# Optimization experiments

Measured on AMD Instinct MI355X. Metric: run time of the kernel, lower is better.

Reference implementation:

```python
import jax, jax.numpy as jnp
import numpy as np


def setup_inputs() -> dict:
    key = jax.random.key(0)
    k1, k2 = jax.random.split(key)
    B, L1, L2, D = 64, 1024, 1024, 768
    sent = jax.random.normal(k1, (B, L1, D), dtype=jnp.float32)
    e = jax.random.normal(k2, (B, L2, L1), dtype=jnp.float32)
    return {"sent": sent, "e": e}


def reference(sent, e):
    # Stable softmax over last axis (alignment weights over L1),
    # then weighted pooling of sent: equivalent to es @ sent.
    es = jax.nn.softmax(e, axis=-1)              # [B, L2, L1]
    out = jnp.einsum('bql,bld->bqd', es, sent)   # [B, L2, D]
    return out
```

## Files before the change

kernel.cpp:

```cpp
#include <hip/hip_runtime.h>
#include <hip/hip_bf16.h>


#define B_  64
#define L1_ 1024
#define L2_ 1024
#define D_  768

typedef __attribute__((ext_vector_type(8))) short short8;
typedef __attribute__((ext_vector_type(4))) float f32x4;
typedef __attribute__((ext_vector_type(8))) unsigned short ushort8;
typedef __attribute__((ext_vector_type(4))) unsigned short ushort4v;

static __device__ __forceinline__ unsigned short f2bf(float x) {
  union { float f; unsigned int u; } c; c.f = x;
  unsigned int r = c.u + 0x7FFF + ((c.u >> 16) & 1);
  return (unsigned short)(r >> 16);
}

#define GLOAD(gp, lp) \
  __builtin_amdgcn_global_load_lds((const __attribute__((address_space(1))) char*)(gp), \
                                   (__attribute__((address_space(3))) char*)(lp), 16, 0, 0)

__global__ __launch_bounds__(256) void transpose_cast_kernel(const float* __restrict__ sent,
                                                             unsigned short* __restrict__ sT) {
  __shared__ unsigned short tile[64][66];
  const int b  = blockIdx.z;
  const int l0 = blockIdx.y << 6;
  const int d0 = blockIdx.x << 6;
  const int t  = threadIdx.x;
  const float* sp = sent + ((size_t)b * L1_ + l0) * D_ + d0;
  const int c4 = (t & 15) << 2;
  const int r0 = t >> 4;
#pragma unroll
  for (int p = 0; p < 4; ++p) {
    const int r = r0 + (p << 4);
    float4 v = *reinterpret_cast<const float4*>(sp + (size_t)r * D_ + c4);
    tile[r][c4 + 0] = f2bf(v.x);
    tile[r][c4 + 1] = f2bf(v.y);
    tile[r][c4 + 2] = f2bf(v.z);
    tile[r][c4 + 3] = f2bf(v.w);
  }
  __syncthreads();
  unsigned short* op = sT + ((size_t)b * D_ + d0) * L1_ + l0;
  const int l8  = (t & 7) << 3;
  const int dd0 = t >> 3;
#pragma unroll
  for (int p = 0; p < 2; ++p) {
    const int d = dd0 + (p << 5);
    ushort8 w;
#pragma unroll
    for (int j = 0; j < 8; ++j) w[j] = tile[l8 + j][d];
    *reinterpret_cast<ushort8*>(op + (size_t)d * L1_ + l8) = w;
  }
}

__global__ __launch_bounds__(256) void exp_rows_kernel(const float* __restrict__ e,
                                                       unsigned short* __restrict__ expE,
                                                       float* __restrict__ rsInv) {
  const int t    = threadIdx.x;
  const int lane = t & 63;
  const int wv   = t >> 6;
  const int rowb = blockIdx.x << 4;
#pragma unroll
  for (int i = 0; i < 4; ++i) {
    const int row = rowb + (i << 2) + wv;
    const float* rp = e + (size_t)row * L1_;
    unsigned short* op = expE + (size_t)row * L1_;
    float s = 0.f;
#pragma unroll
    for (int j = 0; j < 4; ++j) {
      float4 v = *reinterpret_cast<const float4*>(rp + j * 256 + lane * 4);
      float e0 = __expf(v.x), e1 = __expf(v.y), e2 = __expf(v.z), e3 = __expf(v.w);
      s += (e0 + e1) + (e2 + e3);
      ushort4v o;
      o[0] = f2bf(e0); o[1] = f2bf(e1); o[2] = f2bf(e2); o[3] = f2bf(e3);
      *reinterpret_cast<ushort4v*>(op + j * 256 + lane * 4) = o;
    }
#pragma unroll
    for (int dd = 1; dd < 64; dd <<= 1) s += __shfl_xor(s, dd);
    if (lane == 0) rsInv[row] = 1.0f / s;
  }
}

#define BM2 256
#define BN2 256
#define BK2 64
#define NT2   (L1_ / BK2)
#define MT2   (L2_ / BM2)
#define NTL2  (D_ / BN2)
#define NWG2  (B_ * MT2 * NTL2)

#define SAU(T, BUF, RR) do { const int _tt = (T) & (NT2 - 1); \
    GLOAD(Asrc2 + (size_t)(RR) * 64 * L1_ + _tt * BK2, \
          &As2[BUF][((RR) * 64 + w * 8) * BK2]); \
    GLOAD(Asrc2 + (size_t)((RR) + 2) * 64 * L1_ + _tt * BK2, \
          &As2[BUF][(((RR) + 2) * 64 + w * 8) * BK2]); \
  } while (0)
#define SBU(T, BUF, RR) do { const int _tt = (T) & (NT2 - 1); \
    GLOAD(Bsrc2 + (size_t)(RR) * 64 * L1_ + _tt * BK2, \
          &Bs2[BUF][((RR) * 64 + w * 8) * BK2]); \
    GLOAD(Bsrc2 + (size_t)((RR) + 1) * 64 * L1_ + _tt * BK2, \
          &Bs2[BUF][(((RR) + 1) * 64 + w * 8) * BK2]); \
  } while (0)

#define PHASE2(RB, RH, KH, PRE, POST) do { \
    PRE \
    short8 a_[4], b_[4]; \
    _Pragma("unroll") \
    for (int ii = 0; ii < 4; ++ii) { \
      const int ra_ = wm * 128 + ((RH) * 4 + ii) * 16 + l15; \
      a_[ii] = *reinterpret_cast<const short8*>( \
          &As2[RB][ra_ * BK2 + ((((KH) * 4 + ksl) ^ (l15 & 7)) << 3)]); \
      const int rb_ = wn * 64 + ii * 16 + l15; \
      b_[ii] = *reinterpret_cast<const short8*>( \
          &Bs2[RB][rb_ * BK2 + ((((KH) * 4 + ksl) ^ (l15 & 7)) << 3)]); \
    } \
    __builtin_amdgcn_sched_barrier(0); \
    __builtin_amdgcn_s_barrier(); \
    asm volatile("s_waitcnt lgkmcnt(0)" ::: "memory"); \
    __builtin_amdgcn_sched_barrier(0); \
    __builtin_amdgcn_s_setprio(1); \
    _Pragma("unroll") \
    for (int ii = 0; ii < 4; ++ii) \
      _Pragma("unroll") \
      for (int jj = 0; jj < 4; ++jj) \
        acc[(RH) * 4 + ii][jj] = __builtin_amdgcn_mfma_f32_16x16x32_bf16( \
            a_[ii], b_[jj], acc[(RH) * 4 + ii][jj], 0, 0, 0); \
    __builtin_amdgcn_s_setprio(0); \
    POST \
    __builtin_amdgcn_sched_barrier(0); \
    __builtin_amdgcn_s_barrier(); \
  } while (0)

#define TILE2(T, RB, SBUF) do { \
    PHASE2(RB, 0, 0, SAU((T) + 1, SBUF, 1);, ;); \
    PHASE2(RB, 0, 1, SBU((T) + 1, SBUF, 0);, ;); \
    PHASE2(RB, 1, 0, SBU((T) + 1, SBUF, 2); SAU((T) + 2, RB, 0);, ;); \
    PHASE2(RB, 1, 1, ;, \
        asm volatile("s_waitcnt vmcnt(2)" ::: "memory"); \
        __builtin_amdgcn_sched_barrier(0);); \
  } while (0)

__global__ __launch_bounds__(512, 2) void gemm2_kernel(const unsigned short* __restrict__ expE,
                                                       const unsigned short* __restrict__ sT,
                                                       const float* __restrict__ rsInv,
                                                       float* __restrict__ out) {
  __shared__ __align__(16) unsigned short As2[2][BM2 * BK2];
  __shared__ __align__(16) unsigned short Bs2[2][BN2 * BK2];
  __shared__ float sArr[BM2];

  const int orig = blockIdx.x;
  const int wgid = (orig & 7) * (NWG2 / 8) + (orig >> 3);
  const int b    = wgid / (MT2 * NTL2);
  const int rem  = wgid % (MT2 * NTL2);
  const int m0   = (rem / NTL2) * BM2;
  const int n0   = (rem % NTL2) * BN2;

  const int t    = threadIdx.x;
  const int lane = t & 63;
  const int w    = t >> 6;
  const int wm   = w >> 2;
  const int wn   = w & 3;
  const int l15  = lane & 15;
  const int ksl  = lane >> 4;

  const int srow  = w * 8 + (lane >> 3);
  const int sslot = (lane & 7) ^ (lane >> 3);
  const unsigned short* Asrc2 = expE + ((size_t)b * L2_ + m0 + srow) * L1_ + sslot * 8;
  const unsigned short* Bsrc2 = sT   + ((size_t)b * D_  + n0 + srow) * L1_ + sslot * 8;

  f32x4 acc[8][4] = {};

  if (t < BM2) sArr[t] = rsInv[(size_t)b * L2_ + m0 + t];
  SAU(0, 0, 0); SAU(0, 0, 1); SBU(0, 0, 0); SBU(0, 0, 2);
  SAU(1, 1, 0);
  asm volatile("s_waitcnt vmcnt(2) lgkmcnt(0)" ::: "memory");
  __builtin_amdgcn_s_barrier();
  __builtin_amdgcn_sched_barrier(0);

#pragma unroll 1
  for (int kt = 0; kt < NT2; kt += 2) {
    TILE2(kt,     0, 1);
    TILE2(kt + 1, 1, 0);
  }

  const int rbase = (lane >> 4) << 2;
  float* Cb = out + ((size_t)b * L2_ + m0 + wm * 128) * D_ + n0 + wn * 64;
#pragma unroll
  for (int i = 0; i < 8; ++i) {
    float inv[4];
#pragma unroll
    for (int r = 0; r < 4; ++r)
      inv[r] = sArr[wm * 128 + i * 16 + rbase + r];
#pragma unroll
    for (int jj = 0; jj < 4; ++jj)
#pragma unroll
      for (int r = 0; r < 4; ++r)
        Cb[(size_t)(i * 16 + rbase + r) * D_ + jj * 16 + l15] = acc[i][jj][r] * inv[r];
  }
}

#define BM 128
#define BN 256
#define BK 32
#define NT    (L1_ / BK)
#define NTILE (D_ / BN)
#define MTILE (L2_ / BM)
#define NWG   (NTILE * MTILE * B_)

#define SW(r) ((((r) >> 2) ^ (r)) & 3)

#define LOADA(T) do { const int _ta = (T) & (NT - 1);                                        \
    aregs[0] = *reinterpret_cast<const float4*>(Ae + (size_t)rA * L1_ + _ta * BK + cA);      \
    aregs[1] = *reinterpret_cast<const float4*>(Ae + (size_t)rA * L1_ + _ta * BK + cA + 4);  \
  } while (0)

#define EXPWRITE(T) do { if ((T) < NT) {                                        \
    unsigned short* Ad_ = &As[(T) & 1][0];                                      \
    float ex_[8];                                                               \
    ex_[0] = __expf(aregs[0].x); ex_[1] = __expf(aregs[0].y);                   \
    ex_[2] = __expf(aregs[0].z); ex_[3] = __expf(aregs[0].w);                   \
    ex_[4] = __expf(aregs[1].x); ex_[5] = __expf(aregs[1].y);                   \
    ex_[6] = __expf(aregs[1].z); ex_[7] = __expf(aregs[1].w);                   \
    psum += ((ex_[0] + ex_[1]) + (ex_[2] + ex_[3]))                             \
          + ((ex_[4] + ex_[5]) + (ex_[6] + ex_[7]));                            \
    ushort8 w0_;                                                                \
    _Pragma("unroll")                                                           \
    for (int q_ = 0; q_ < 8; ++q_) w0_[q_] = f2bf(ex_[q_]);                     \
    *reinterpret_cast<ushort8*>(&Ad_[rA * BK + aslot * 8]) = w0_;               \
  } } while (0)

#define SB(T) do { if ((T) < NT) {                                              \
    GLOAD(Bb + (size_t)rB0 * L1_ + (T) * BK + sB0, &Bs[(T) & 1][(w * 32) * BK]);      \
    GLOAD(Bb + (size_t)rB1 * L1_ + (T) * BK + sB1, &Bs[(T) & 1][(w * 32 + 16) * BK]); \
  } } while (0)

__global__ __launch_bounds__(512, 2) void gemm_fused_kernel(const float* __restrict__ e,
                                                            const unsigned short* __restrict__ sT,
                                                            float* __restrict__ out) {
  __shared__ __align__(16) unsigned short As[2][BM * BK];
  __shared__ __align__(16) unsigned short Bs[2][BN * BK];
  __shared__ float sArr[BM];

  const int orig = blockIdx.x;
  const int wgid = (orig & 7) * (NWG / 8) + (orig >> 3);
  const int b    = wgid / (NTILE * MTILE);
  const int rem  = wgid % (NTILE * MTILE);
  const int m0   = (rem / NTILE) * BM;
  const int n0   = (rem % NTILE) * BN;

  const int t    = threadIdx.x;
  const int lane = t & 63;
  const int w    = t >> 6;
  const int wm   = w >> 2;
  const int wn   = w & 3;
  const int l15  = lane & 15;
  const int ksl  = lane >> 4;
  const int rA   = w * 16 + (lane >> 2);
  const int cA   = (lane & 3) * 8;
  const int aslot = (lane & 3) ^ SW(rA);
  const int rB0  = w * 32 + (lane >> 2);
  const int rB1  = rB0 + 16;
  const int sB0  = ((lane & 3) ^ SW(rB0)) * 8;
  const int sB1  = ((lane & 3) ^ SW(rB1)) * 8;

  const float*          Ae = e  + ((size_t)b * L2_ + m0) * L1_;
  const unsigned short* Bb = sT + ((size_t)b * D_  + n0) * L1_;

  f32x4 acc[4][4] = {};
  float4 aregs[2];
  float psum = 0.f;

  LOADA(0);
  SB(0);
  EXPWRITE(0);
  LOADA(1);
  asm volatile("s_waitcnt vmcnt(2) lgkmcnt(0)" ::: "memory");
  __builtin_amdgcn_s_barrier();
  __builtin_amdgcn_sched_barrier(0);

  for (int kt = 0; kt < NT; ++kt) {
    SB(kt + 1);
    EXPWRITE(kt + 1);
    LOADA(kt + 2);

    const unsigned short* Apt = As[kt & 1];
    const unsigned short* Bpt = Bs[kt & 1];
    short8 a[4], bb[4];
    __builtin_amdgcn_s_setprio(1);
#pragma unroll
    for (int i = 0; i < 4; ++i) {
      const int ra = wm * 64 + i * 16 + l15;
      a[i] = *reinterpret_cast<const short8*>(&Apt[ra * BK + ((ksl ^ SW(ra)) << 3)]);
      const int rb = wn * 64 + i * 16 + l15;
      bb[i] = *reinterpret_cast<const short8*>(&Bpt[rb * BK + ((ksl ^ SW(rb)) << 3)]);
    }
#pragma unroll
    for (int i = 0; i < 4; ++i)
#pragma unroll
      for (int jn = 0; jn < 4; ++jn)
        acc[i][jn] = __builtin_amdgcn_mfma_f32_16x16x32_bf16(a[i], bb[jn], acc[i][jn], 0, 0, 0);
    __builtin_amdgcn_s_setprio(0);

    if (kt < NT - 1) {
      asm volatile("s_waitcnt vmcnt(2) lgkmcnt(0)" ::: "memory");
      __builtin_amdgcn_s_barrier();
      __builtin_amdgcn_sched_barrier(0);
    }
  }

  psum += __shfl_xor(psum, 1);
  psum += __shfl_xor(psum, 2);
  if ((lane & 3) == 0) sArr[rA] = psum;
  __syncthreads();

  const int rbase = (lane >> 4) << 2;
  float* Cb = out + ((size_t)b * L2_ + m0 + wm * 64) * D_ + n0 + wn * 64;
#pragma unroll
  for (int i = 0; i < 4; ++i) {
    float inv[4];
#pragma unroll
    for (int r = 0; r < 4; ++r)
      inv[r] = 1.0f / sArr[wm * 64 + i * 16 + rbase + r];
#pragma unroll
    for (int jn = 0; jn < 4; ++jn)
#pragma unroll
      for (int r = 0; r < 4; ++r)
        Cb[(size_t)(i * 16 + rbase + r) * D_ + jn * 16 + l15] = acc[i][jn][r] * inv[r];
  }
}

extern "C" void kernel_launch(void* const* d_in, const int* in_sizes, int n_in,
                              void* d_out, int out_size, void* d_ws, size_t ws_size,
                              hipStream_t stream) {
  const float* sent = (const float*)d_in[0];
  const float* e    = (const float*)d_in[1];
  float* out = (float*)d_out;

  const size_t ST_BYTES   = (size_t)B_ * D_ * L1_ * 2;
  const size_t EXPE_BYTES = (size_t)B_ * L2_ * L1_ * 2;
  const size_t RS_BYTES   = (size_t)B_ * L2_ * 4;

  unsigned short* sT = (unsigned short*)d_ws;

  transpose_cast_kernel<<<dim3(D_ / 64, L1_ / 64, B_), 256, 0, stream>>>(sent, sT);

  if (ws_size >= ST_BYTES + EXPE_BYTES + RS_BYTES) {
    unsigned short* expE  = (unsigned short*)((char*)d_ws + ST_BYTES);
    float*          rsInv = (float*)((char*)d_ws + ST_BYTES + EXPE_BYTES);
    exp_rows_kernel<<<dim3(B_ * L2_ / 16), 256, 0, stream>>>(e, expE, rsInv);
    gemm2_kernel<<<dim3(NWG2), 512, 0, stream>>>(expE, sT, rsInv, out);
  } else {
    gemm_fused_kernel<<<dim3(NWG), 512, 0, stream>>>(e, sT, out);
  }
}
```

Before: 302.5 us.

## Merge prep kernels into one launch and restructure GEMM main-loop pipeline

New measurement: 289.4 us. 1.05x faster.

```diff
diff --git a/kernel.cpp b/kernel.cpp
--- a/kernel.cpp
+++ b/kernel.cpp
@@ -21,6 +21,198 @@
 #define GLOAD(gp, lp) \
   __builtin_amdgcn_global_load_lds((const __attribute__((address_space(1))) char*)(gp), \
                                    (__attribute__((address_space(3))) char*)(lp), 16, 0, 0)
+
+#define TC_BLOCKS (12 * 16 * 64)
+__global__ __launch_bounds__(256) void prep_kernel(const float* __restrict__ sent,
+                                                   const float* __restrict__ e,
+                                                   unsigned short* __restrict__ sT,
+                                                   unsigned short* __restrict__ expE,
+                                                   float* __restrict__ rsInv) {
+  __shared__ unsigned short tile[64][66];
+  const int bid = blockIdx.x;
+  const int t   = threadIdx.x;
+  if (bid < TC_BLOCKS) {
+    const int b  = bid / 192;
+    const int r2 = bid % 192;
+    const int l0 = (r2 / 12) << 6;
+    const int d0 = (r2 % 12) << 6;
+    const float* sp = sent + ((size_t)b * L1_ + l0) * D_ + d0;
+    const int c4 = (t & 15) << 2;
+    const int r0 = t >> 4;
+#pragma unroll
+    for (int p = 0; p < 4; ++p) {
+      const int r = r0 + (p << 4);
+      float4 v = *reinterpret_cast<const float4*>(sp + (size_t)r * D_ + c4);
+      tile[r][c4 + 0] = f2bf(v.x);
+      tile[r][c4 + 1] = f2bf(v.y);
+      tile[r][c4 + 2] = f2bf(v.z);
+      tile[r][c4 + 3] = f2bf(v.w);
+    }
+    __syncthreads();
+    unsigned short* op = sT + ((size_t)b * D_ + d0) * L1_ + l0;
+    const int l8  = (t & 7) << 3;
+    const int dd0 = t >> 3;
+#pragma unroll
+    for (int p = 0; p < 2; ++p) {
+      const int d = dd0 + (p << 5);
+      ushort8 w;
+#pragma unroll
+      for (int j = 0; j < 8; ++j) w[j] = tile[l8 + j][d];
+      *reinterpret_cast<ushort8*>(op + (size_t)d * L1_ + l8) = w;
+    }
+  } else {
+    const int lane = t & 63;
+    const int wv   = t >> 6;
+    const int rowb = (bid - TC_BLOCKS) << 4;
+#pragma unroll
+    for (int i = 0; i < 4; ++i) {
+      const int row = rowb + (i << 2) + wv;
+      const float* rp = e + (size_t)row * L1_;
+      unsigned short* op = expE + (size_t)row * L1_;
+      float s = 0.f;
+#pragma unroll
+      for (int j = 0; j < 4; ++j) {
+        float4 v = *reinterpret_cast<const float4*>(rp + j * 256 + lane * 4);
+        float e0 = __expf(v.x), e1 = __expf(v.y), e2 = __expf(v.z), e3 = __expf(v.w);
+        s += (e0 + e1) + (e2 + e3);
+        ushort4v o;
+        o[0] = f2bf(e0); o[1] = f2bf(e1); o[2] = f2bf(e2); o[3] = f2bf(e3);
+        *reinterpret_cast<ushort4v*>(op + j * 256 + lane * 4) = o;
+      }
+#pragma unroll
+      for (int dd = 1; dd < 64; dd <<= 1) s += __shfl_xor(s, dd);
+      if (lane == 0) rsInv[row] = 1.0f / s;
+    }
+  }
+}
+
+#define BM2 256
+#define BN2 256
+#define BK2 64
+#define NT2   (L1_ / BK2)
+#define MT2   (L2_ / BM2)
+#define NTL2  (D_ / BN2)
+#define NWG2  (B_ * MT2 * NTL2)
+
+#define SAU(T, BUF, RR) do { const int _tt = (T) & (NT2 - 1); \
+    GLOAD(Asrc2 + (size_t)(RR) * 64 * L1_ + _tt * BK2, \
+          &As2[BUF][((RR) * 64 + w * 8) * BK2]); \
+    GLOAD(Asrc2 + (size_t)((RR) + 2) * 64 * L1_ + _tt * BK2, \
+          &As2[BUF][(((RR) + 2) * 64 + w * 8) * BK2]); \
+  } while (0)
+#define SBN(T, BUF, NH) do { const int _tt = (T) & (NT2 - 1); \
+    { const int _b0 = ((w) >> 2) * 64 + (NH) * 32 + ((w) & 3) * 8; \
+      GLOAD(BsrcS + (size_t)_b0 * L1_ + _tt * BK2, &Bs2[BUF][_b0 * BK2]); } \
+    { const int _g1 = 8 + w; \
+      const int _b1 = (_g1 >> 2) * 64 + (NH) * 32 + (_g1 & 3) * 8; \
+      GLOAD(BsrcS + (size_t)_b1 * L1_ + _tt * BK2, &Bs2[BUF][_b1 * BK2]); } \
+  } while (0)
+
+#define CKPT do { \
+    asm volatile("s_waitcnt vmcnt(4)" ::: "memory"); \
+    __builtin_amdgcn_s_barrier(); \
+  } while (0)
+
+#define PHASE3(RB, RH, NH, RDB, PRE, POST) do { \
+    PRE \
+    if (RDB) { \
+      _Pragma("unroll") \
+      for (int jj = 0; jj < 2; ++jj) { \
+        const int rb_ = wn * 64 + (NH) * 32 + jj * 16 + l15; \
+        _Pragma("unroll") \
+        for (int kk = 0; kk < 2; ++kk) \
+          b_[jj][kk] = *reinterpret_cast<const short8*>( \
+              &Bs2[RB][rb_ * BK2 + (((kk * 4 + ksl) ^ (l15 & 7)) << 3)]); \
+      } \
+    } \
+    short8 a_[4][2]; \
+    _Pragma("unroll") \
+    for (int ii = 0; ii < 4; ++ii) { \
+      const int ra_ = wm * 128 + ((RH) * 4 + ii) * 16 + l15; \
+      _Pragma("unroll") \
+      for (int kk = 0; kk < 2; ++kk) \
+        a_[ii][kk] = *reinterpret_cast<const short8*>( \
+            &As2[RB][ra_ * BK2 + (((kk * 4 + ksl) ^ (l15 & 7)) << 3)]); \
+    } \
+    asm volatile("s_waitcnt lgkmcnt(0)" ::: "memory"); \
+    __builtin_amdgcn_sched_barrier(0); \
+    __builtin_amdgcn_s_setprio(1); \
+    _Pragma("unroll") \
+    for (int kk = 0; kk < 2; ++kk) \
+      _Pragma("unroll") \
+      for (int ii = 0; ii < 4; ++ii) \
+        _Pragma("unroll") \
+        for (int jj = 0; jj < 2; ++jj) \
+          acc[(RH) * 4 + ii][(NH) * 2 + jj] = __builtin_amdgcn_mfma_f32_16x16x32_bf16( \
+              a_[ii][kk], b_[jj][kk], acc[(RH) * 4 + ii][(NH) * 2 + jj], 0, 0, 0); \
+    __builtin_amdgcn_s_setprio(0); \
+    POST \
+  } while (0)
+
+#define TILE3(T, RB) do { \
+    PHASE3(RB, 0, 0, 1, SAU((T) + 1, (RB) ^ 1, 0);, CKPT;); \
+    PHASE3(RB, 1, 0, 0, SBN((T) + 1, (RB) ^ 1, 0);, CKPT;); \
+    PHASE3(RB, 1, 1, 1, SAU((T) + 1, (RB) ^ 1, 1);, ;); \
+    PHASE3(RB, 0, 1, 0, SBN((T) + 1, (RB) ^ 1, 1);, CKPT;); \
+  } while (0)
+
+__global__ __launch_bounds__(512, 2) void gemm2_kernel(const unsigned short* __restrict__ expE,
+                                                       const unsigned short* __restrict__ sT,
+                                                       const float* __restrict__ rsInv,
+                                                       float* __restrict__ out) {
+  __shared__ __align__(16) unsigned short As2[2][BM2 * BK2];
+  __shared__ __align__(16) unsigned short Bs2[2][BN2 * BK2];
+  __shared__ float sArr[BM2];
+
+  const int orig = blockIdx.x;
+  const int wgid = (orig & 7) * (NWG2 / 8) + (orig >> 3);
+  const int b    = wgid / (MT2 * NTL2);
+  const int rem  = wgid % (MT2 * NTL2);
+  const int m0   = (rem / NTL2) * BM2;
+  const int n0   = (rem % NTL2) * BN2;
+
+  const int t    = threadIdx.x;
+  const int lane = t & 63;
+  const int w    = t >> 6;
+  const int wm   = w >> 2;
+  const int wn   = w & 3;
+  const int l15  = lane & 15;
+  const int ksl  = lane >> 4;
+
+  const int sslot = (lane & 7) ^ (lane >> 3);
+  const unsigned short* Asrc2 = expE + ((size_t)b * L2_ + m0 + w * 8 + (lane >> 3)) * L1_ + sslot * 8;
+  const unsigned short* BsrcS = sT   + ((size_t)b * D_  + n0 + (lane >> 3)) * L1_ + sslot * 8;
+
+  f32x4 acc[8][4] = {};
+  short8 b_[2][2];
+
+  if (t < BM2) sArr[t] = rsInv[(size_t)b * L2_ + m0 + t];
+  SAU(0, 0, 0); SAU(0, 0, 1); SBN(0, 0, 0); SBN(0, 0, 1);
+  asm volatile("s_waitcnt vmcnt(0) lgkmcnt(0)" ::: "memory");
+  __builtin_amdgcn_s_barrier();
+
+#pragma unroll 1
+  for (int kt = 0; kt < NT2; kt += 2) {
+    TILE3(kt,     0);
+    TILE3(kt + 1, 1);
+  }
+  asm volatile("s_waitcnt vmcnt(0)" ::: "memory");
+
+  const int rbase = (lane >> 4) << 2;
+  float* Cb = out + ((size_t)b * L2_ + m0 + wm * 128) * D_ + n0 + wn * 64;
+#pragma unroll
+  for (int i = 0; i < 8; ++i) {
+    float inv[4];
+#pragma unroll
+    for (int r = 0; r < 4; ++r)
+      inv[r] = sArr[wm * 128 + i * 16 + rbase + r];
+#pragma unroll
+    for (int jj = 0; jj < 4; ++jj)
+#pragma unroll
+      for (int r = 0; r < 4; ++r)
+        Cb[(size_t)(i * 16 + rbase + r) * D_ + jj * 16 + l15] = acc[i][jj][r] * inv[r];
+  }
+}
 
 __global__ __launch_bounds__(256) void transpose_cast_kernel(const float* __restrict__ sent,
                                                              unsigned short* __restrict__ sT) {
@@ -52,152 +244,6 @@
 #pragma unroll
     for (int j = 0; j < 8; ++j) w[j] = tile[l8 + j][d];
     *reinterpret_cast<ushort8*>(op + (size_t)d * L1_ + l8) = w;
-  }
-}
-
-__global__ __launch_bounds__(256) void exp_rows_kernel(const float* __restrict__ e,
-                                                       unsigned short* __restrict__ expE,
-                                                       float* __restrict__ rsInv) {
-  const int t    = threadIdx.x;
-  const int lane = t & 63;
-  const int wv   = t >> 6;
-  const int rowb = blockIdx.x << 4;
-#pragma unroll
-  for (int i = 0; i < 4; ++i) {
-    const int row = rowb + (i << 2) + wv;
-    const float* rp = e + (size_t)row * L1_;
-    unsigned short* op = expE + (size_t)row * L1_;
-    float s = 0.f;
-#pragma unroll
-    for (int j = 0; j < 4; ++j) {
-      float4 v = *reinterpret_cast<const float4*>(rp + j * 256 + lane * 4);
-      float e0 = __expf(v.x), e1 = __expf(v.y), e2 = __expf(v.z), e3 = __expf(v.w);
-      s += (e0 + e1) + (e2 + e3);
-      ushort4v o;
-      o[0] = f2bf(e0); o[1] = f2bf(e1); o[2] = f2bf(e2); o[3] = f2bf(e3);
-      *reinterpret_cast<ushort4v*>(op + j * 256 + lane * 4) = o;
-    }
-#pragma unroll
-    for (int dd = 1; dd < 64; dd <<= 1) s += __shfl_xor(s, dd);
-    if (lane == 0) rsInv[row] = 1.0f / s;
-  }
-}
-
-#define BM2 256
-#define BN2 256
-#define BK2 64
-#define NT2   (L1_ / BK2)
-#define MT2   (L2_ / BM2)
-#define NTL2  (D_ / BN2)
-#define NWG2  (B_ * MT2 * NTL2)
-
-#define SAU(T, BUF, RR) do { const int _tt = (T) & (NT2 - 1); \
-    GLOAD(Asrc2 + (size_t)(RR) * 64 * L1_ + _tt * BK2, \
-          &As2[BUF][((RR) * 64 + w * 8) * BK2]); \
-    GLOAD(Asrc2 + (size_t)((RR) + 2) * 64 * L1_ + _tt * BK2, \
-          &As2[BUF][(((RR) + 2) * 64 + w * 8) * BK2]); \
-  } while (0)
-#define SBU(T, BUF, RR) do { const int _tt = (T) & (NT2 - 1); \
-    GLOAD(Bsrc2 + (size_t)(RR) * 64 * L1_ + _tt * BK2, \
-          &Bs2[BUF][((RR) * 64 + w * 8) * BK2]); \
-    GLOAD(Bsrc2 + (size_t)((RR) + 1) * 64 * L1_ + _tt * BK2, \
-          &Bs2[BUF][(((RR) + 1) * 64 + w * 8) * BK2]); \
-  } while (0)
-
-#define PHASE2(RB, RH, KH, PRE, POST) do { \
-    PRE \
-    short8 a_[4], b_[4]; \
-    _Pragma("unroll") \
-    for (int ii = 0; ii < 4; ++ii) { \
-      const int ra_ = wm * 128 + ((RH) * 4 + ii) * 16 + l15; \
-      a_[ii] = *reinterpret_cast<const short8*>( \
-          &As2[RB][ra_ * BK2 + ((((KH) * 4 + ksl) ^ (l15 & 7)) << 3)]); \
-      const int rb_ = wn * 64 + ii * 16 + l15; \
-      b_[ii] = *reinterpret_cast<const short8*>( \
-          &Bs2[RB][rb_ * BK2 + ((((KH) * 4 + ksl) ^ (l15 & 7)) << 3)]); \
-    } \
-    __builtin_amdgcn_sched_barrier(0); \
-    __builtin_amdgcn_s_barrier(); \
-    asm volatile("s_waitcnt lgkmcnt(0)" ::: "memory"); \
-    __builtin_amdgcn_sched_barrier(0); \
-    __builtin_amdgcn_s_setprio(1); \
-    _Pragma("unroll") \
-    for (int ii = 0; ii < 4; ++ii) \
-      _Pragma("unroll") \
-      for (int jj = 0; jj < 4; ++jj) \
-        acc[(RH) * 4 + ii][jj] = __builtin_amdgcn_mfma_f32_16x16x32_bf16( \
-            a_[ii], b_[jj], acc[(RH) * 4 + ii][jj], 0, 0, 0); \
-    __builtin_amdgcn_s_setprio(0); \
-    POST \
-    __builtin_amdgcn_sched_barrier(0); \
-    __builtin_amdgcn_s_barrier(); \
-  } while (0)
-
-#define TILE2(T, RB, SBUF) do { \
-    PHASE2(RB, 0, 0, SAU((T) + 1, SBUF, 1);, ;); \
-    PHASE2(RB, 0, 1, SBU((T) + 1, SBUF, 0);, ;); \
-    PHASE2(RB, 1, 0, SBU((T) + 1, SBUF, 2); SAU((T) + 2, RB, 0);, ;); \
-    PHASE2(RB, 1, 1, ;, \
-        asm volatile("s_waitcnt vmcnt(2)" ::: "memory"); \
-        __builtin_amdgcn_sched_barrier(0);); \
-  } while (0)
-
-__global__ __launch_bounds__(512, 2) void gemm2_kernel(const unsigned short* __restrict__ expE,
-                                                       const unsigned short* __restrict__ sT,
-                                                       const float* __restrict__ rsInv,
-                                                       float* __restrict__ out) {
-  __shared__ __align__(16) unsigned short As2[2][BM2 * BK2];
-  __shared__ __align__(16) unsigned short Bs2[2][BN2 * BK2];
-  __shared__ float sArr[BM2];
-
-  const int orig = blockIdx.x;
-  const int wgid = (orig & 7) * (NWG2 / 8) + (orig >> 3);
-  const int b    = wgid / (MT2 * NTL2);
-  const int rem  = wgid % (MT2 * NTL2);
-  const int m0   = (rem / NTL2) * BM2;
-  const int n0   = (rem % NTL2) * BN2;
-
-  const int t    = threadIdx.x;
-  const int lane = t & 63;
-  const int w    = t >> 6;
-  const int wm   = w >> 2;
-  const int wn   = w & 3;
-  const int l15  = lane & 15;
-  const int ksl  = lane >> 4;
-
-  const int srow  = w * 8 + (lane >> 3);
-  const int sslot = (lane & 7) ^ (lane >> 3);
-  const unsigned short* Asrc2 = expE + ((size_t)b * L2_ + m0 + srow) * L1_ + sslot * 8;
-  const unsigned short* Bsrc2 = sT   + ((size_t)b * D_  + n0 + srow) * L1_ + sslot * 8;
-
-  f32x4 acc[8][4] = {};
-
-  if (t < BM2) sArr[t] = rsInv[(size_t)b * L2_ + m0 + t];
-  SAU(0, 0, 0); SAU(0, 0, 1); SBU(0, 0, 0); SBU(0, 0, 2);
-  SAU(1, 1, 0);
-  asm volatile("s_waitcnt vmcnt(2) lgkmcnt(0)" ::: "memory");
-  __builtin_amdgcn_s_barrier();
-  __builtin_amdgcn_sched_barrier(0);
-
-#pragma unroll 1
-  for (int kt = 0; kt < NT2; kt += 2) {
-    TILE2(kt,     0, 1);
-    TILE2(kt + 1, 1, 0);
-  }
-
-  const int rbase = (lane >> 4) << 2;
-  float* Cb = out + ((size_t)b * L2_ + m0 + wm * 128) * D_ + n0 + wn * 64;
-#pragma unroll
-  for (int i = 0; i < 8; ++i) {
-    float inv[4];
-#pragma unroll
-    for (int r = 0; r < 4; ++r)
-      inv[r] = sArr[wm * 128 + i * 16 + rbase + r];
-#pragma unroll
-    for (int jj = 0; jj < 4; ++jj)
-#pragma unroll
-      for (int r = 0; r < 4; ++r)
-        Cb[(size_t)(i * 16 + rbase + r) * D_ + jj * 16 + l15] = acc[i][jj][r] * inv[r];
   }
 }
 
@@ -231,7 +277,7 @@
     *reinterpret_cast<ushort8*>(&Ad_[rA * BK + aslot * 8]) = w0_;               \
   } } while (0)
 
-#define SB(T) do { if ((T) < NT) {                                              \
+#define SBF(T) do { if ((T) < NT) {                                             \
     GLOAD(Bb + (size_t)rB0 * L1_ + (T) * BK + sB0, &Bs[(T) & 1][(w * 32) * BK]);      \
     GLOAD(Bb + (size_t)rB1 * L1_ + (T) * BK + sB1, &Bs[(T) & 1][(w * 32 + 16) * BK]); \
   } } while (0)
@@ -273,7 +319,7 @@
   float psum = 0.f;
 
   LOADA(0);
-  SB(0);
+  SBF(0);
   EXPWRITE(0);
   LOADA(1);
   asm volatile("s_waitcnt vmcnt(2) lgkmcnt(0)" ::: "memory");
@@ -281,7 +327,7 @@
   __builtin_amdgcn_sched_barrier(0);
 
   for (int kt = 0; kt < NT; ++kt) {
-    SB(kt + 1);
+    SBF(kt + 1);
     EXPWRITE(kt + 1);
     LOADA(kt + 2);
 
@@ -344,14 +390,13 @@
 
   unsigned short* sT = (unsigned short*)d_ws;
 
-  transpose_cast_kernel<<<dim3(D_ / 64, L1_ / 64, B_), 256, 0, stream>>>(sent, sT);
-
   if (ws_size >= ST_BYTES + EXPE_BYTES + RS_BYTES) {
     unsigned short* expE  = (unsigned short*)((char*)d_ws + ST_BYTES);
     float*          rsInv = (float*)((char*)d_ws + ST_BYTES + EXPE_BYTES);
-    exp_rows_kernel<<<dim3(B_ * L2_ / 16), 256, 0, stream>>>(e, expE, rsInv);
+    prep_kernel<<<dim3(TC_BLOCKS + B_ * L2_ / 16), 256, 0, stream>>>(sent, e, sT, expE, rsInv);
     gemm2_kernel<<<dim3(NWG2), 512, 0, stream>>>(expE, sT, rsInv, out);
   } else {
+    transpose_cast_kernel<<<dim3(D_ / 64, L1_ / 64, B_), 256, 0, stream>>>(sent, sT);
     gemm_fused_kernel<<<dim3(NWG), 512, 0, stream>>>(e, sT, out);
   }
 }
```
